# Kernel optimization log

Measured on AMD Instinct MI355X. Metric: run time of the kernel, lower is better.

Reference implementation:

```python
import jax, jax.numpy as jnp
import numpy as np

P = 4       # primitives
NF = 36     # non-functor cats (depth <= 1)
NEG = -1e9  # safe -inf
B, N, V, D = 32, 32, 32000, 64


def _build_functor_tables():
    # cat ids: 0..3 primitives; 4..35 depth-1 functors op(res,arg) res,arg<4;
    # remaining: depth-2 functors op(res,arg), res,arg in nf cats, not both primitive.
    def d1(op, res, arg):
        return 4 + op * 16 + res * 4 + arg
    nxt = NF
    d2 = {}
    for op in range(2):
        for res in range(NF):
            for arg in range(NF):
                if res < P and arg < P:
                    continue
                d2[(op, res, arg)] = nxt
                nxt += 1
    C = nxt  # 2596
    def fid(op, res, arg):
        return d1(op, res, arg) if (res < P and arg < P) else d2[(op, res, arg)]
    lf = np.zeros((NF, NF), np.int32)
    rf = np.zeros((NF, NF), np.int32)
    for res in range(NF):
        for arg in range(NF):
            lf[arg, res] = fid(0, res, arg)  # '-b' : functor on the left
            rf[arg, res] = fid(1, res, arg)  # '-a' : functor on the right
    return lf, rf, C


def setup_inputs() -> dict:
    lf, rf, C = _build_functor_tables()
    key = jax.random.key(0)
    ks = jax.random.split(key, 24)
    g = lambda i, shp, s: jax.random.normal(ks[i], shp, dtype=jnp.float32) * s
    inp = {
        "x": jax.random.randint(ks[0], (B, N), 0, V, dtype=jnp.int32),
        "l_functors": jnp.asarray(lf),
        "r_functors": jnp.asarray(rf),
        "root_W": g(1, (1, C), 0.1),
        "root_b": g(2, (C,), 0.1),
        "rule_W": g(3, (NF, 2 * NF), 0.1),
        "rule_b": g(4, (2 * NF,), 0.1),
        "nt_emb": g(5, (C, D), 1.0),
        "sW1": g(6, (D, D), 0.125), "sb1": g(7, (D,), 0.02),
        "r1W1": g(8, (D, D), 0.125), "r1b1": g(9, (D,), 0.02),
        "r1W2": g(10, (D, D), 0.125), "r1b2": g(11, (D,), 0.02),
        "r2W1": g(12, (D, D), 0.125), "r2b1": g(13, (D,), 0.02),
        "r2W2": g(14, (D, D), 0.125), "r2b2": g(15, (D,), 0.02),
        "sW2": g(16, (D, 2), 0.125), "sb2": g(17, (2,), 0.02),
        "vocab_W": g(18, (D, V), 0.125), "vocab_b": g(19, (V,), 0.02),
    }
    return inp


def _res_layer(h, W1, b1, W2, b2):
    return jax.nn.relu(jax.nn.relu(h @ W1 + b1) @ W2 + b2) + h


def reference(x, l_functors, r_functors, root_W, root_b, rule_W, rule_b, nt_emb,
              sW1, sb1, r1W1, r1b1, r1W2, r1b2, r2W1, r2b1, r2W2, r2b2,
              sW2, sb2, vocab_W, vocab_b):
    C = nt_emb.shape[0]
    # --- grammar parameters ---
    root_mask = jnp.where(jnp.arange(C) < P, 0.0, NEG)
    root_scores = jax.nn.log_softmax(root_mask + (root_W[0] + root_b))      # [C]
    rule_scores = jax.nn.log_softmax(rule_W + rule_b, axis=1)               # [NF,2NF] (rule_mlp(eye))
    h = nt_emb @ sW1 + sb1
    h = _res_layer(h, r1W1, r1b1, r1W2, r1b2)
    h = _res_layer(h, r2W1, r2b1, r2W2, r2b2)
    split = jax.nn.log_softmax(h @ sW2 + sb2, axis=1)                       # [C,2]
    G_larg = rule_scores[:, :NF] + split[:NF, 0:1]                          # [res,arg]
    G_rarg = rule_scores[:, NF:] + split[:NF, 0:1]
    # --- emission (word model): log_softmax over vocab, gather word ids ---
    dist = jax.nn.log_softmax(nt_emb @ vocab_W + vocab_b, axis=1)           # [C,V]
    emis = dist[:, x]                                                       # [C,B,N]
    beta1 = jnp.transpose(emis, (2, 1, 0)) + split[:, 1]                    # [N,B,C] lexical inside
    # --- CKY inside algorithm ---
    n = beta1.shape[0]
    lf_c = jnp.minimum(l_functors, NF - 1); l_valid = l_functors < NF
    rf_c = jnp.minimum(r_functors, NF - 1); r_valid = r_functors < NF
    rf1 = beta1[:, :, r_functors]   # [N,B,arg,res] functor score at length-1 spans
    lf1 = beta1[:, :, l_functors]
    Gl = G_larg.T                   # [arg,res]
    Gr = G_rarg.T
    chart = {1: beta1[:, :, :NF]}   # chart[L][i] = inside of span [i, i+L) over nf cats
    for L in range(2, n + 1):
        S = n - L + 1
        terms = []
        for k in range(1, L):  # left length k, right length L-k
            left = chart[k][:S]              # [S,B,NF]
            right = chart[L - k][k:k + S]    # [S,B,NF]
            # case larg: res -> arg (left, nf) + r_functor (right)
            if L - k == 1:
                rF = rf1[k:k + S]
            else:
                rF = jnp.where(r_valid, right[..., rf_c], NEG)
            tA = left[..., :, None] + rF + Gl                       # [S,B,arg,res]
            # case rarg: res -> l_functor (left) + arg (right, nf)
            if k == 1:
                lF = lf1[:S]
            else:
                lF = jnp.where(l_valid, left[..., lf_c], NEG)
            tB = right[..., :, None] + lF + Gr
            terms.append(jax.nn.logsumexp(jnp.concatenate([tA, tB], axis=2), axis=2))
        chart[L] = jax.nn.logsumexp(jnp.stack(terms, 0), axis=0)    # [S,B,NF]
    top = chart[n][0]                                               # [B,NF]
    logprob = jax.nn.logsumexp(top + root_scores[:NF], axis=-1)     # root mask keeps primitives only
    return -logprob
```

## Files before the change

kernel.cpp:

```cpp
#include <hip/hip_runtime.h>
#include <hip/hip_bf16.h>
#include <math.h>

#define CT 2596
#define NF36 36
#define BB 32
#define NN 32
#define VV 32000
#define DD 64
#define NEGF -1e9f
#define NVT 2000

typedef __attribute__((ext_vector_type(8))) short bf16x8;
typedef __attribute__((ext_vector_type(4))) float f32x4;

__device__ __forceinline__ uint32_t f2bf_bits(float x) {
  union { float f; uint32_t u; } v; v.f = x;
  return (v.u + 0x7FFFu + ((v.u >> 16) & 1u)) >> 16;
}
__device__ __forceinline__ float bflo(uint32_t u) {
  union { uint32_t u; float f; } v; v.u = u << 16; return v.f;
}
__device__ __forceinline__ float bfhi(uint32_t u) {
  union { uint32_t u; float f; } v; v.u = u & 0xFFFF0000u; return v.f;
}

__global__ __launch_bounds__(256) void k_mlp(
    const float* __restrict__ nt_emb,
    const float* __restrict__ sW1, const float* __restrict__ sb1,
    const float* __restrict__ r1W1, const float* __restrict__ r1b1,
    const float* __restrict__ r1W2, const float* __restrict__ r1b2,
    const float* __restrict__ r2W1, const float* __restrict__ r2b1,
    const float* __restrict__ r2W2, const float* __restrict__ r2b2,
    const float* __restrict__ sW2, const float* __restrict__ sb2,
    float* __restrict__ split0, float* __restrict__ split1) {
  int tid = threadIdx.x;
  int rl = tid >> 6, j = tid & 63;
  int c = blockIdx.x * 4 + rl;
  __shared__ float hs[4][64], ts[4][64];

  ts[rl][j] = nt_emb[(size_t)c * 64 + j];
  __syncthreads();
  float a = sb1[j];
  for (int i = 0; i < 64; i++) a += ts[rl][i] * sW1[i * 64 + j];
  __syncthreads();
  hs[rl][j] = a;
  __syncthreads();
  float u = r1b1[j];
  for (int i = 0; i < 64; i++) u += hs[rl][i] * r1W1[i * 64 + j];
  u = fmaxf(u, 0.f);
  ts[rl][j] = u;
  __syncthreads();
  float w = r1b2[j];
  for (int i = 0; i < 64; i++) w += ts[rl][i] * r1W2[i * 64 + j];
  w = fmaxf(w, 0.f) + hs[rl][j];
  __syncthreads();
  hs[rl][j] = w;
  __syncthreads();
  u = r2b1[j];
  for (int i = 0; i < 64; i++) u += hs[rl][i] * r2W1[i * 64 + j];
  u = fmaxf(u, 0.f);
  ts[rl][j] = u;
  __syncthreads();
  w = r2b2[j];
  for (int i = 0; i < 64; i++) w += ts[rl][i] * r2W2[i * 64 + j];
  w = fmaxf(w, 0.f) + hs[rl][j];
  __syncthreads();
  hs[rl][j] = w;
  __syncthreads();
  if (j < 2) {
    float o = sb2[j];
    for (int i = 0; i < 64; i++) o += hs[rl][i] * sW2[i * 2 + j];
    ts[rl][j] = o;
  }
  __syncthreads();
  if (j < 2) {
    float o0 = ts[rl][0], o1 = ts[rl][1];
    float mx = fmaxf(o0, o1);
    float l = mx + __logf(__expf(o0 - mx) + __expf(o1 - mx));
    if (j == 0) split0[c] = o0 - l;
    else        split1[c] = o1 - l;
  }
}

__global__ __launch_bounds__(256) void k_prelim(
    const float* __restrict__ rule_W, const float* __restrict__ rule_b,
    const float* __restrict__ root_W, const float* __restrict__ root_b,
    const float* __restrict__ split0,
    float* __restrict__ Gl, float* __restrict__ Gr, float* __restrict__ root36,
    float* __restrict__ lseacc) {
  __shared__ float rs[36 * 72];
  __shared__ float lse4s;
  int tid = threadIdx.x;
  for (int i = tid; i < CT; i += 256) lseacc[i] = 0.f;
  if (tid < 36) {
    float mx = -1e30f;
    for (int q = 0; q < 72; q++) mx = fmaxf(mx, rule_W[tid * 72 + q] + rule_b[q]);
    float ss = 0.f;
    for (int q = 0; q < 72; q++) ss += __expf(rule_W[tid * 72 + q] + rule_b[q] - mx);
    float l = mx + __logf(ss);
    for (int q = 0; q < 72; q++) rs[tid * 72 + q] = rule_W[tid * 72 + q] + rule_b[q] - l;
  }
  if (tid == 0) {
    float mx = -1e30f;
    for (int i = 0; i < 4; i++) mx = fmaxf(mx, root_W[i] + root_b[i]);
    float ss = 0.f;
    for (int i = 0; i < 4; i++) ss += __expf(root_W[i] + root_b[i] - mx);
    lse4s = mx + __logf(ss);
  }
  __syncthreads();
  if (tid < 36)
    root36[tid] = ((tid < 4) ? 0.f : NEGF) + root_W[tid] + root_b[tid] - lse4s;
  for (int i = tid; i < 1296; i += 256) {
    int arg = i / 36, res = i - arg * 36;
    float s0 = split0[res];
    Gl[i] = rs[res * 72 + arg] + s0;
    Gr[i] = rs[res * 72 + 36 + arg] + s0;
  }
}

__global__ __launch_bounds__(256) void k_cvt_w(
    const float* __restrict__ vocab_W, uint4* __restrict__ Wt) {
  int g = blockIdx.x * 256 + threadIdx.x;
  if (g >= NVT * 128) return;
  int l = g & 63;
  int f = (g >> 6) & 1;
  int vt = g >> 7;
  int v = vt * 16 + (l & 15);
  int kb = f * 32 + 8 * (l >> 4);
  uint32_t d[4];
#pragma unroll
  for (int p = 0; p < 4; p++) {
    float a = vocab_W[(size_t)(kb + 2 * p) * VV + v];
    float b = vocab_W[(size_t)(kb + 2 * p + 1) * VV + v];
    d[p] = f2bf_bits(a) | (f2bf_bits(b) << 16);
  }
  uint4 o; o.x = d[0]; o.y = d[1]; o.z = d[2]; o.w = d[3];
  Wt[g] = o;
}

__global__ __launch_bounds__(256) void k_gather_tok(
    const float* __restrict__ vocab_W, const float* __restrict__ vocab_b,
    const int* __restrict__ x, uint4* __restrict__ Bt, float* __restrict__ vbt) {
  int g = blockIdx.x * 256 + threadIdx.x;
  if (g >= 8192) return;
  int l = g & 63, kf = (g >> 6) & 1, t = g >> 7;
  int j = t * 16 + (l & 15);
  int tok = x[j];
  int kb = kf * 32 + 8 * (l >> 4);
  uint32_t d[4];
#pragma unroll
  for (int p = 0; p < 4; p++) {
    float a = vocab_W[(size_t)(kb + 2 * p) * VV + tok];
    float b = vocab_W[(size_t)(kb + 2 * p + 1) * VV + tok];
    d[p] = f2bf_bits(a) | (f2bf_bits(b) << 16);
  }
  uint4 o; o.x = d[0]; o.y = d[1]; o.z = d[2]; o.w = d[3];
  Bt[g] = o;
  if (g < 1024) vbt[g] = vocab_b[x[g]];
}

__global__ __launch_bounds__(256) void k_lse_mfma(
    const float* __restrict__ nt_emb, const uint4* __restrict__ Wt,
    const float* __restrict__ vocab_b, float* __restrict__ lseacc) {
  int tid = threadIdx.x;
  int w = tid >> 6, l = tid & 63;
  int c0 = blockIdx.y * 128;
  int lrow = l & 15, lgrp = l >> 4;

  bf16x8 A[8][2];
#pragma unroll
  for (int ct = 0; ct < 8; ct++) {
    int row = c0 + ct * 16 + lrow;
#pragma unroll
    for (int kf = 0; kf < 2; kf++) {
      bf16x8 fr;
      if (row < CT) {
        const float4* src = (const float4*)(nt_emb + (size_t)row * 64 + kf * 32 + lgrp * 8);
        float4 s0 = src[0], s1 = src[1];
        fr[0] = (short)f2bf_bits(s0.x); fr[1] = (short)f2bf_bits(s0.y);
        fr[2] = (short)f2bf_bits(s0.z); fr[3] = (short)f2bf_bits(s0.w);
        fr[4] = (short)f2bf_bits(s1.x); fr[5] = (short)f2bf_bits(s1.y);
        fr[6] = (short)f2bf_bits(s1.z); fr[7] = (short)f2bf_bits(s1.w);
      } else {
#pragma unroll
        for (int e = 0; e < 8; e++) fr[e] = 0;
      }
      A[ct][kf] = fr;
    }
  }

  float sums[8][4];
#pragma unroll
  for (int ct = 0; ct < 8; ct++)
#pragma unroll
    for (int i = 0; i < 4; i++) sums[ct][i] = 0.f;

  int t0 = blockIdx.x * 80;
  for (int t = t0 + w; t < t0 + 80; t += 4) {
    union { uint4 u; bf16x8 h; } b0, b1;
    b0.u = Wt[(size_t)(t * 2) * 64 + l];
    b1.u = Wt[(size_t)(t * 2 + 1) * 64 + l];
    float vb = vocab_b[t * 16 + lrow];
#pragma unroll
    for (int ct = 0; ct < 8; ct++) {
      f32x4 acc = {0.f, 0.f, 0.f, 0.f};
      acc = __builtin_amdgcn_mfma_f32_16x16x32_bf16(A[ct][0], b0.h, acc, 0, 0, 0);
      acc = __builtin_amdgcn_mfma_f32_16x16x32_bf16(A[ct][1], b1.h, acc, 0, 0, 0);
#pragma unroll
      for (int i = 0; i < 4; i++) sums[ct][i] += __expf(acc[i] + vb);
    }
  }

#pragma unroll
  for (int ct = 0; ct < 8; ct++)
#pragma unroll
    for (int i = 0; i < 4; i++) {
      float v = sums[ct][i];
      v += __shfl_xor(v, 1);
      v += __shfl_xor(v, 2);
      v += __shfl_xor(v, 4);
      v += __shfl_xor(v, 8);
      sums[ct][i] = v;
    }
  if (lrow == 0) {
#pragma unroll
    for (int ct = 0; ct < 8; ct++)
#pragma unroll
      for (int i = 0; i < 4; i++) {
        int row = c0 + ct * 16 + lgrp * 4 + i;
        if (row < CT) atomicAdd(&lseacc[row], sums[ct][i]);
      }
  }
}

__global__ __launch_bounds__(256) void k_beta1_mfma(
    const float* __restrict__ nt_emb, const uint4* __restrict__ Bt,
    const float* __restrict__ vbt, const float* __restrict__ lseacc,
    const float* __restrict__ split1, float* __restrict__ beta1) {
  int tid = threadIdx.x;
  int w = tid >> 6, l = tid & 63;
  int c0 = blockIdx.x * 64;
  int lrow = l & 15, lgrp = l >> 4;
  __shared__ float addS[64];
  if (tid < 64) {
    int row = c0 + tid;
    addS[tid] = (row < CT) ? (split1[row] - __logf(lseacc[row])) : 0.f;
  }

  bf16x8 A[4][2];
#pragma unroll
  for (int ct = 0; ct < 4; ct++) {
    int row = c0 + ct * 16 + lrow;
#pragma unroll
    for (int kf = 0; kf < 2; kf++) {
      bf16x8 fr;
      if (row < CT) {
        const float4* src = (const float4*)(nt_emb + (size_t)row * 64 + kf * 32 + lgrp * 8);
        float4 s0 = src[0], s1 = src[1];
        fr[0] = (short)f2bf_bits(s0.x); fr[1] = (short)f2bf_bits(s0.y);
        fr[2] = (short)f2bf_bits(s0.z); fr[3] = (short)f2bf_bits(s0.w);
        fr[4] = (short)f2bf_bits(s1.x); fr[5] = (short)f2bf_bits(s1.y);
        fr[6] = (short)f2bf_bits(s1.z); fr[7] = (short)f2bf_bits(s1.w);
      } else {
#pragma unroll
        for (int e = 0; e < 8; e++) fr[e] = 0;
      }
      A[ct][kf] = fr;
    }
  }
  __syncthreads();
  float addv[4][4];
#pragma unroll
  for (int ct = 0; ct < 4; ct++)
#pragma unroll
    for (int i = 0; i < 4; i++) addv[ct][i] = addS[ct * 16 + lgrp * 4 + i];

  for (int t = w; t < 64; t += 4) {
    union { uint4 u; bf16x8 h; } b0, b1;
    b0.u = Bt[t * 128 + l];
    b1.u = Bt[t * 128 + 64 + l];
    int j = t * 16 + lrow;
    float vb = vbt[j];
    int jc = (j & 31) * 32 + (j >> 5);
    float* outb = beta1 + (size_t)jc * CT;
#pragma unroll
    for (int ct = 0; ct < 4; ct++) {
      f32x4 acc = {0.f, 0.f, 0.f, 0.f};
      acc = __builtin_amdgcn_mfma_f32_16x16x32_bf16(A[ct][0], b0.h, acc, 0, 0, 0);
      acc = __builtin_amdgcn_mfma_f32_16x16x32_bf16(A[ct][1], b1.h, acc, 0, 0, 0);
      int r0 = c0 + ct * 16 + lgrp * 4;
      if (r0 + 3 < CT) {
        float4 o;
        o.x = acc[0] + vb + addv[ct][0];
        o.y = acc[1] + vb + addv[ct][1];
        o.z = acc[2] + vb + addv[ct][2];
        o.w = acc[3] + vb + addv[ct][3];
        *(float4*)(outb + r0) = o;
      } else {
        for (int i = 0; i < 4; i++)
          if (r0 + i < CT) outb[r0 + i] = acc[i] + vb + addv[ct][i];
      }
    }
  }
}

__global__ __launch_bounds__(256) void k_edge(
    const float* __restrict__ beta1, const int* __restrict__ lf_t,
    const int* __restrict__ rf_t, const float* __restrict__ Gl,
    const float* __restrict__ Gr,
    uint32_t* __restrict__ elB, uint32_t* __restrict__ erB) {
  int sb = blockIdx.x;
  const float* brow = beta1 + (size_t)sb * CT;
  size_t ob = (size_t)sb * 720;
  for (int wd = threadIdx.x; wd < 720; wd += 256) {
    int res = wd / 20, p = wd - res * 20;
    int a0 = 2 * p, a1 = 2 * p + 1;
    uint32_t l0 = 0, l1 = 0, r0 = 0, r1 = 0;
    if (a0 < 36) {
      int i0 = a0 * 36 + res;
      l0 = f2bf_bits(__expf(brow[lf_t[i0]] + Gr[i0]));
      r0 = f2bf_bits(__expf(brow[rf_t[i0]] + Gl[i0]));
    }
    if (a1 < 36) {
      int i1 = a1 * 36 + res;
      l1 = f2bf_bits(__expf(brow[lf_t[i1]] + Gr[i1]));
      r1 = f2bf_bits(__expf(brow[rf_t[i1]] + Gl[i1]));
    }
    elB[ob + wd] = l0 | (l1 << 16);
    erB[ob + wd] = r0 | (r1 << 16);
  }
}

__global__ __launch_bounds__(1024, 4) void k_cky(
    const float* __restrict__ beta1, const uint32_t* __restrict__ elB,
    const uint32_t* __restrict__ erB, const float* __restrict__ Gl,
    const float* __restrict__ Gr, const float* __restrict__ root36,
    float* __restrict__ out) {
  __shared__ __align__(16) float D[19008];
  __shared__ float Mt[528];
  __shared__ __align__(16) float PA[1280], PB[1280];
  __shared__ __align__(16) float Ec1lT[512], Ec1rT[512];
  __shared__ __align__(16) float eGlT[16], eGrT[16];
  __shared__ unsigned int candb[2][33];
  __shared__ float MIDacc[128];

  int b = blockIdx.x, tid = threadIdx.x;

  if (tid < 66) candb[tid / 33][tid % 33] = 0u;
  if (tid < 32) Mt[tid] = 0.f;
  if (tid < 16) {
    int res = tid >> 2, a = tid & 3;
    eGlT[tid] = __expf(Gl[a * 36 + res]);
    eGrT[tid] = __expf(Gr[a * 36 + res]);
  }
  for (int i = tid; i < 1280; i += 1024) { PA[i] = 0.f; PB[i] = 0.f; }
  __syncthreads();
  for (int i = tid; i < 32 * 36; i += 1024) {
    int s = i / 36;
    float v = __expf(beta1[(size_t)(s * 32 + b) * CT + (i - s * 36)]);
    D[i] = v;
    atomicMax(&candb[1][s], __float_as_uint(v));
  }
  __syncthreads();
  for (int i = tid; i < 512; i += 1024) {
    int s = i >> 4, rr = (i >> 2) & 3, a = i & 3;
    float d1 = D[s * 36 + a];
    Ec1lT[i] = d1 * eGlT[rr * 4 + a];
    Ec1rT[i] = d1 * eGrT[rr * 4 + a];
  }
  __syncthreads();

  for (int L = 2; L <= 32; L++) {
    int S = 33 - L;
    int offL  = 36 * (((L - 1) * (66 - L)) >> 1);
    int offP  = 36 * (((L - 2) * (67 - L)) >> 1);
    int offML = ((L - 1) * (66 - L)) >> 1;
    int offMP = ((L - 2) * (67 - L)) >> 1;
    int par = L & 1, parP = par ^ 1;

    if (tid < 33) candb[par][tid] = 0u;
    if (tid >= 64 && tid < 192) MIDacc[tid - 64] = 0.f;
    int totA = S * 36;
    for (int o = tid; o < totA; o += 1024) {
      int s = o / 36, j = o - s * 36;
      float MtA = Mt[offMP + s], MtB = Mt[offMP + s + 1];
      float cA = MtA + __logf(fmaxf(__uint_as_float(candb[parP][s]), 1e-37f));
      float cB = MtB + __logf(fmaxf(__uint_as_float(candb[parP][s + 1]), 1e-37f));
      float Mn = fmaxf(cA, cB);
      PA[s * 40 + j] = D[offP + s * 36 + j] * __expf(MtA - Mn);
      PB[s * 40 + j] = D[offP + (s + 1) * 36 + j] * __expf(MtB - Mn);
      if (j == 0) Mt[offML + s] = Mn;
    }
    __syncthreads();

    int tot = S * 36;
    int nmid = (L >= 4) ? 4 * S * (L - 3) : 0;
    int W = tot + nmid;
    for (int o = tid; o < W; o += 1024) {
      if (o < tot) {
        int s = o / 36, res = o - s * 36;
        const uint4* el4 = (const uint4*)(elB + (size_t)(s * 32 + b) * 720 + res * 20);
        const uint4* er4 = (const uint4*)(erB + (size_t)((s + L - 1) * 32 + b) * 720 + res * 20);
        const float4* pB4 = (const float4*)(PB + s * 40);
        const float4* pA4 = (const float4*)(PA + s * 40);
        float a0 = 0.f, a1 = 0.f, a2 = 0.f, a3 = 0.f;
#pragma unroll
        for (int q = 0; q < 5; q++) {
          uint4 u = el4[q];
          float4 p0 = pB4[2 * q], p1 = pB4[2 * q + 1];
          a0 = fmaf(bflo(u.x), p0.x, a0); a1 = fmaf(bfhi(u.x), p0.y, a1);
          a2 = fmaf(bflo(u.y), p0.z, a2); a3 = fmaf(bfhi(u.y), p0.w, a3);
          a0 = fmaf(bflo(u.z), p1.x, a0); a1 = fmaf(bfhi(u.z), p1.y, a1);
          a2 = fmaf(bflo(u.w), p1.z, a2); a3 = fmaf(bfhi(u.w), p1.w, a3);
          uint4 v = er4[q];
          float4 q0 = pA4[2 * q], q1 = pA4[2 * q + 1];
          a0 = fmaf(bflo(v.x), q0.x, a0); a1 = fmaf(bfhi(v.x), q0.y, a1);
          a2 = fmaf(bflo(v.y), q0.z, a2); a3 = fmaf(bfhi(v.y), q0.w, a3);
          a0 = fmaf(bflo(v.z), q1.x, a0); a1 = fmaf(bfhi(v.z), q1.y, a1);
          a2 = fmaf(bflo(v.w), q1.z, a2); a3 = fmaf(bfhi(v.w), q1.w, a3);
        }
        if (res < 4 && L >= 3) {
          const float4* ecl = (const float4*)(Ec1lT + s * 16 + res * 4);
          const float4* ecr = (const float4*)(Ec1rT + (s + L - 1) * 16 + res * 4);
          float4 e0 = ecl[0], pb = pB4[5 + res];
          float4 e1 = ecr[0], pa = pA4[1 + res];
          a0 = fmaf(e0.x, pb.x, a0); a1 = fmaf(e0.y, pb.y, a1);
          a2 = fmaf(e0.z, pb.z, a2); a3 = fmaf(e0.w, pb.w, a3);
          a0 = fmaf(e1.x, pa.x, a0); a1 = fmaf(e1.y, pa.y, a1);
          a2 = fmaf(e1.z, pa.z, a2); a3 = fmaf(e1.w, pa.w, a3);
        }
        float val = (a0 + a1) + (a2 + a3);
        D[offL + o] = val;
        atomicMax(&candb[par][s], __float_as_uint(val));
      } else {
        int o2 = o - tot;
        int kidx = o2 / (4 * S);
        int rem = o2 - kidx * 4 * S;
        int s = rem >> 2, res = rem & 3;
        int k = kidx + 2;
        int lk = L - k;
        int tk = ((k - 1) * (66 - k)) >> 1;
        int tl = ((lk - 1) * (66 - lk)) >> 1;
        const float4* Dk4 = (const float4*)(D + 36 * tk + s * 36);
        const float4* Dl4 = (const float4*)(D + 36 * tl + (s + k) * 36);
        float4 dk0 = Dk4[0], dkh = Dk4[1 + res];
        float4 dl0 = Dl4[0], dlh = Dl4[5 + res];
        float4 egl = ((const float4*)eGlT)[res];
        float4 egr = ((const float4*)eGrT)[res];
        float f = __expf(Mt[tk + s] + Mt[tl + s + k] - Mt[offML + s]);
        float sub = dk0.x * dlh.x * egl.x + dk0.y * dlh.y * egl.y
                  + dk0.z * dlh.z * egl.z + dk0.w * dlh.w * egl.w
                  + dl0.x * dkh.x * egr.x + dl0.y * dkh.y * egr.y
                  + dl0.z * dkh.z * egr.z + dl0.w * dkh.w * egr.w;
        atomicAdd(&MIDacc[rem], f * sub);
      }
    }
    __syncthreads();

    if (L >= 4) {
      for (int o = tid; o < 4 * S; o += 1024) {
        int s = o >> 2;
        float nv = D[offL + s * 36 + (o & 3)] + MIDacc[o];
        D[offL + s * 36 + (o & 3)] = nv;
        atomicMax(&candb[par][s], __float_as_uint(nv));
      }
    }
    __syncthreads();
  }

  int wid = tid >> 6, lane = tid & 63;
  if (wid == 0) {
    int off32 = 36 * ((31 * 34) >> 1);
    float v = (lane < 36) ? D[off32 + lane] * __expf(root36[lane]) : 0.f;
#pragma unroll
    for (int w = 32; w > 0; w >>= 1) v += __shfl_xor(v, w);
    if (lane == 0) out[b] = -(Mt[527] + __logf(v));
  }
}

extern "C" void kernel_launch(void* const* d_in, const int* in_sizes, int n_in,
                              void* d_out, int out_size, void* d_ws, size_t ws_size,
                              hipStream_t stream) {
  const int*   x       = (const int*)d_in[0];
  const int*   lf_t    = (const int*)d_in[1];
  const int*   rf_t    = (const int*)d_in[2];
  const float* root_W  = (const float*)d_in[3];
  const float* root_b  = (const float*)d_in[4];
  const float* rule_W  = (const float*)d_in[5];
  const float* rule_b  = (const float*)d_in[6];
  const float* nt_emb  = (const float*)d_in[7];
  const float* sW1     = (const float*)d_in[8];
  const float* sb1     = (const float*)d_in[9];
  const float* r1W1    = (const float*)d_in[10];
  const float* r1b1    = (const float*)d_in[11];
  const float* r1W2    = (const float*)d_in[12];
  const float* r1b2    = (const float*)d_in[13];
  const float* r2W1    = (const float*)d_in[14];
  const float* r2b1    = (const float*)d_in[15];
  const float* r2W2    = (const float*)d_in[16];
  const float* r2b2    = (const float*)d_in[17];
  const float* sW2     = (const float*)d_in[18];
  const float* sb2     = (const float*)d_in[19];
  const float* vocab_W = (const float*)d_in[20];
  const float* vocab_b = (const float*)d_in[21];
  float* outp = (float*)d_out;

  float* ws = (float*)d_ws;
  float* split0 = ws;
  float* split1 = ws + 2596;
  float* Gl     = ws + 5192;
  float* Gr     = ws + 6488;
  float* root36 = ws + 7784;
  float* lseacc = ws + 7848;
  float* vbt    = ws + 10448;
  float* beta1  = ws + 11472;
  uint32_t* elB = (uint32_t*)(ws + 2669776);
  uint32_t* erB = (uint32_t*)(ws + 3407056);
  uint4* Wt     = (uint4*)(ws + 2669776);
  uint4* Bt     = (uint4*)(ws + 4144336);

  k_mlp<<<649, 256, 0, stream>>>(nt_emb, sW1, sb1, r1W1, r1b1, r1W2, r1b2,
                                 r2W1, r2b1, r2W2, r2b2, sW2, sb2, split0, split1);
  k_prelim<<<1, 256, 0, stream>>>(rule_W, rule_b, root_W, root_b, split0,
                                  Gl, Gr, root36, lseacc);
  k_cvt_w<<<1000, 256, 0, stream>>>(vocab_W, Wt);
  k_gather_tok<<<32, 256, 0, stream>>>(vocab_W, vocab_b, x, Bt, vbt);
  k_lse_mfma<<<dim3(25, 21), 256, 0, stream>>>(nt_emb, Wt, vocab_b, lseacc);
  k_beta1_mfma<<<41, 256, 0, stream>>>(nt_emb, Bt, vbt, lseacc, split1, beta1);
  k_edge<<<1024, 256, 0, stream>>>(beta1, lf_t, rf_t, Gl, Gr, elB, erB);
  k_cky<<<32, 1024, 0, stream>>>(beta1, elB, erB, Gl, Gr, root36, outp);
}
```

Before: 228.4 us.

## Parallelize prelim, merge prep kernels, split beta1 grid, defer CKY mid-term fold

k_prelim is spread over 37 blocks, one per rule row plus one for the root, instead of running in a single block. The weight-convert, token-gather and lseacc-zeroing kernels are merged into one launch, and k_beta1_mfma gets an 8-way grid split over token tiles. In k_cky the separate pass that folds MIDacc into the chart is removed: the fold now happens lazily in the next length's normalisation step, using double-buffered MIDacc and a compact C4 copy of primitive cells, which drops one block-wide barrier per span length. The edge-weight loads are also prefetched into registers before the first barrier, at the cost of extra register pressure and more complex max tracking.

```diff
diff --git a/kernel.cpp b/kernel.cpp
--- a/kernel.cpp
+++ b/kernel.cpp
@@ -83,81 +83,88 @@
   }
 }
 
-__global__ __launch_bounds__(256) void k_prelim(
+__global__ __launch_bounds__(128) void k_prelim(
     const float* __restrict__ rule_W, const float* __restrict__ rule_b,
     const float* __restrict__ root_W, const float* __restrict__ root_b,
     const float* __restrict__ split0,
-    float* __restrict__ Gl, float* __restrict__ Gr, float* __restrict__ root36,
+    float* __restrict__ Gl, float* __restrict__ Gr, float* __restrict__ root36) {
+  int tid = threadIdx.x;
+  int blk = blockIdx.x;
+  if (blk < 36) {
+    int res = blk;
+    __shared__ float red[4];
+    float v = (tid < 72) ? rule_W[res * 72 + tid] + rule_b[tid] : -1e30f;
+    float m = v;
+#pragma unroll
+    for (int w = 32; w > 0; w >>= 1) m = fmaxf(m, __shfl_xor(m, w));
+    if ((tid & 63) == 0) red[tid >> 6] = m;
+    __syncthreads();
+    m = fmaxf(red[0], red[1]);
+    float e = (tid < 72) ? __expf(v - m) : 0.f;
+#pragma unroll
+    for (int w = 32; w > 0; w >>= 1) e += __shfl_xor(e, w);
+    if ((tid & 63) == 0) red[2 + (tid >> 6)] = e;
+    __syncthreads();
+    float l = m + __logf(red[2] + red[3]);
+    if (tid < 36) {
+      float s0 = split0[res];
+      Gl[tid * 36 + res] = rule_W[res * 72 + tid] + rule_b[tid] - l + s0;
+      Gr[tid * 36 + res] = rule_W[res * 72 + 36 + tid] + rule_b[36 + tid] - l + s0;
+    }
+  } else {
+    __shared__ float lse4s;
+    if (tid == 0) {
+      float mx = -1e30f;
+      for (int i = 0; i < 4; i++) mx = fmaxf(mx, root_W[i] + root_b[i]);
+      float ss = 0.f;
+      for (int i = 0; i < 4; i++) ss += __expf(root_W[i] + root_b[i] - mx);
+      lse4s = mx + __logf(ss);
+    }
+    __syncthreads();
+    if (tid < 36)
+      root36[tid] = ((tid < 4) ? 0.f : NEGF) + root_W[tid] + root_b[tid] - lse4s;
+  }
+}
+
+__global__ __launch_bounds__(256) void k_prep(
+    const float* __restrict__ vocab_W, const float* __restrict__ vocab_b,
+    const int* __restrict__ x, uint4* __restrict__ Wt,
+    uint4* __restrict__ Bt, float* __restrict__ vbt,
     float* __restrict__ lseacc) {
-  __shared__ float rs[36 * 72];
-  __shared__ float lse4s;
-  int tid = threadIdx.x;
-  for (int i = tid; i < CT; i += 256) lseacc[i] = 0.f;
-  if (tid < 36) {
-    float mx = -1e30f;
-    for (int q = 0; q < 72; q++) mx = fmaxf(mx, rule_W[tid * 72 + q] + rule_b[q]);
-    float ss = 0.f;
-    for (int q = 0; q < 72; q++) ss += __expf(rule_W[tid * 72 + q] + rule_b[q] - mx);
-    float l = mx + __logf(ss);
-    for (int q = 0; q < 72; q++) rs[tid * 72 + q] = rule_W[tid * 72 + q] + rule_b[q] - l;
-  }
-  if (tid == 0) {
-    float mx = -1e30f;
-    for (int i = 0; i < 4; i++) mx = fmaxf(mx, root_W[i] + root_b[i]);
-    float ss = 0.f;
-    for (int i = 0; i < 4; i++) ss += __expf(root_W[i] + root_b[i] - mx);
-    lse4s = mx + __logf(ss);
-  }
-  __syncthreads();
-  if (tid < 36)
-    root36[tid] = ((tid < 4) ? 0.f : NEGF) + root_W[tid] + root_b[tid] - lse4s;
-  for (int i = tid; i < 1296; i += 256) {
-    int arg = i / 36, res = i - arg * 36;
-    float s0 = split0[res];
-    Gl[i] = rs[res * 72 + arg] + s0;
-    Gr[i] = rs[res * 72 + 36 + arg] + s0;
-  }
-}
-
-__global__ __launch_bounds__(256) void k_cvt_w(
-    const float* __restrict__ vocab_W, uint4* __restrict__ Wt) {
-  int g = blockIdx.x * 256 + threadIdx.x;
-  if (g >= NVT * 128) return;
-  int l = g & 63;
-  int f = (g >> 6) & 1;
-  int vt = g >> 7;
-  int v = vt * 16 + (l & 15);
-  int kb = f * 32 + 8 * (l >> 4);
-  uint32_t d[4];
-#pragma unroll
-  for (int p = 0; p < 4; p++) {
-    float a = vocab_W[(size_t)(kb + 2 * p) * VV + v];
-    float b = vocab_W[(size_t)(kb + 2 * p + 1) * VV + v];
-    d[p] = f2bf_bits(a) | (f2bf_bits(b) << 16);
-  }
-  uint4 o; o.x = d[0]; o.y = d[1]; o.z = d[2]; o.w = d[3];
-  Wt[g] = o;
-}
-
-__global__ __launch_bounds__(256) void k_gather_tok(
-    const float* __restrict__ vocab_W, const float* __restrict__ vocab_b,
-    const int* __restrict__ x, uint4* __restrict__ Bt, float* __restrict__ vbt) {
-  int g = blockIdx.x * 256 + threadIdx.x;
-  if (g >= 8192) return;
-  int l = g & 63, kf = (g >> 6) & 1, t = g >> 7;
-  int j = t * 16 + (l & 15);
-  int tok = x[j];
-  int kb = kf * 32 + 8 * (l >> 4);
-  uint32_t d[4];
-#pragma unroll
-  for (int p = 0; p < 4; p++) {
-    float a = vocab_W[(size_t)(kb + 2 * p) * VV + tok];
-    float b = vocab_W[(size_t)(kb + 2 * p + 1) * VV + tok];
-    d[p] = f2bf_bits(a) | (f2bf_bits(b) << 16);
-  }
-  uint4 o; o.x = d[0]; o.y = d[1]; o.z = d[2]; o.w = d[3];
-  Bt[g] = o;
-  if (g < 1024) vbt[g] = vocab_b[x[g]];
+  int blk = blockIdx.x;
+  if (blk < 1000) {
+    int g = blk * 256 + threadIdx.x;
+    int l = g & 63, f = (g >> 6) & 1, vt = g >> 7;
+    int v = vt * 16 + (l & 15);
+    int kb = f * 32 + 8 * (l >> 4);
+    uint32_t d[4];
+#pragma unroll
+    for (int p = 0; p < 4; p++) {
+      float a = vocab_W[(size_t)(kb + 2 * p) * VV + v];
+      float b = vocab_W[(size_t)(kb + 2 * p + 1) * VV + v];
+      d[p] = f2bf_bits(a) | (f2bf_bits(b) << 16);
+    }
+    uint4 o; o.x = d[0]; o.y = d[1]; o.z = d[2]; o.w = d[3];
+    Wt[g] = o;
+  } else if (blk < 1032) {
+    int g = (blk - 1000) * 256 + threadIdx.x;
+    int l = g & 63, kf = (g >> 6) & 1, t = g >> 7;
+    int j = t * 16 + (l & 15);
+    int tok = x[j];
+    int kb = kf * 32 + 8 * (l >> 4);
+    uint32_t d[4];
+#pragma unroll
+    for (int p = 0; p < 4; p++) {
+      float a = vocab_W[(size_t)(kb + 2 * p) * VV + tok];
+      float b = vocab_W[(size_t)(kb + 2 * p + 1) * VV + tok];
+      d[p] = f2bf_bits(a) | (f2bf_bits(b) << 16);
+    }
+    uint4 o; o.x = d[0]; o.y = d[1]; o.z = d[2]; o.w = d[3];
+    Bt[g] = o;
+    if (g < 1024) vbt[g] = vocab_b[x[g]];
+  } else {
+    for (int i = threadIdx.x; i < CT; i += 256) lseacc[i] = 0.f;
+  }
 }
 
 __global__ __launch_bounds__(256) void k_lse_mfma(
@@ -276,7 +283,8 @@
 #pragma unroll
     for (int i = 0; i < 4; i++) addv[ct][i] = addS[ct * 16 + lgrp * 4 + i];
 
-  for (int t = w; t < 64; t += 4) {
+  int t0 = blockIdx.y * 8;
+  for (int t = t0 + w; t < t0 + 8; t += 4) {
     union { uint4 u; bf16x8 h; } b0, b1;
     b0.u = Bt[t * 128 + l];
     b1.u = Bt[t * 128 + 64 + l];
@@ -338,12 +346,13 @@
     const float* __restrict__ Gr, const float* __restrict__ root36,
     float* __restrict__ out) {
   __shared__ __align__(16) float D[19008];
+  __shared__ __align__(16) float C4[2116];
   __shared__ float Mt[528];
   __shared__ __align__(16) float PA[1280], PB[1280];
   __shared__ __align__(16) float Ec1lT[512], Ec1rT[512];
   __shared__ __align__(16) float eGlT[16], eGrT[16];
   __shared__ unsigned int candb[2][33];
-  __shared__ float MIDacc[128];
+  __shared__ float MIDacc[2][128];
 
   int b = blockIdx.x, tid = threadIdx.x;
 
@@ -372,48 +381,81 @@
   __syncthreads();
 
   for (int L = 2; L <= 32; L++) {
-    int S = 33 - L;
-    int offL  = 36 * (((L - 1) * (66 - L)) >> 1);
-    int offP  = 36 * (((L - 2) * (67 - L)) >> 1);
-    int offML = ((L - 1) * (66 - L)) >> 1;
-    int offMP = ((L - 2) * (67 - L)) >> 1;
-    int par = L & 1, parP = par ^ 1;
+    const int S = 33 - L;
+    const int offL  = 36 * (((L - 1) * (66 - L)) >> 1);
+    const int offP  = 36 * (((L - 2) * (67 - L)) >> 1);
+    const int offML = ((L - 1) * (66 - L)) >> 1;
+    const int offMP = ((L - 2) * (67 - L)) >> 1;
+    const int par = L & 1, parP = par ^ 1;
+    const int tot = S * 36;
+    const int nmid = (L >= 4) ? 4 * S * (L - 3) : 0;
+    const int W = tot + nmid;
+
+    uint4 pl[5], pr[5];
+    if (tid < tot) {
+      int s = tid / 36, res = tid - s * 36;
+      const uint4* el4 = (const uint4*)(elB + (size_t)(s * 32 + b) * 720 + res * 20);
+      const uint4* er4 = (const uint4*)(erB + (size_t)((s + L - 1) * 32 + b) * 720 + res * 20);
+#pragma unroll
+      for (int q = 0; q < 5; q++) { pl[q] = el4[q]; pr[q] = er4[q]; }
+    }
 
     if (tid < 33) candb[par][tid] = 0u;
-    if (tid >= 64 && tid < 192) MIDacc[tid - 64] = 0.f;
-    int totA = S * 36;
-    for (int o = tid; o < totA; o += 1024) {
+    if (tid >= 512 && tid < 640) MIDacc[par][tid - 512] = 0.f;
+    const float* MIDp = MIDacc[parP];
+    for (int o = tid; o < tot; o += 1024) {
       int s = o / 36, j = o - s * 36;
       float MtA = Mt[offMP + s], MtB = Mt[offMP + s + 1];
-      float cA = MtA + __logf(fmaxf(__uint_as_float(candb[parP][s]), 1e-37f));
-      float cB = MtB + __logf(fmaxf(__uint_as_float(candb[parP][s + 1]), 1e-37f));
+      float dA = D[offP + s * 36 + j];
+      float dB = D[offP + (s + 1) * 36 + j];
+      if (L >= 5 && j < 4) { dA += MIDp[s * 4 + j]; dB += MIDp[(s + 1) * 4 + j]; }
+      if (j < 4) {
+        C4[(offMP + s) * 4 + j] = dA;
+        if (s == S - 1) C4[(offMP + s + 1) * 4 + j] = dB;
+      }
+      float mA = __uint_as_float(candb[parP][s]);
+      float mB = __uint_as_float(candb[parP][s + 1]);
+      if (L >= 5) {
+#pragma unroll
+        for (int j2 = 0; j2 < 4; j2++) {
+          mA = fmaxf(mA, D[offP + s * 36 + j2] + MIDp[s * 4 + j2]);
+          mB = fmaxf(mB, D[offP + (s + 1) * 36 + j2] + MIDp[(s + 1) * 4 + j2]);
+        }
+      }
+      float cA = MtA + __logf(fmaxf(mA, 1e-37f));
+      float cB = MtB + __logf(fmaxf(mB, 1e-37f));
       float Mn = fmaxf(cA, cB);
-      PA[s * 40 + j] = D[offP + s * 36 + j] * __expf(MtA - Mn);
-      PB[s * 40 + j] = D[offP + (s + 1) * 36 + j] * __expf(MtB - Mn);
+      PA[s * 40 + j] = dA * __expf(MtA - Mn);
+      PB[s * 40 + j] = dB * __expf(MtB - Mn);
       if (j == 0) Mt[offML + s] = Mn;
     }
     __syncthreads();
 
-    int tot = S * 36;
-    int nmid = (L >= 4) ? 4 * S * (L - 3) : 0;
-    int W = tot + nmid;
     for (int o = tid; o < W; o += 1024) {
       if (o < tot) {
         int s = o / 36, res = o - s * 36;
-        const uint4* el4 = (const uint4*)(elB + (size_t)(s * 32 + b) * 720 + res * 20);
-        const uint4* er4 = (const uint4*)(erB + (size_t)((s + L - 1) * 32 + b) * 720 + res * 20);
+        uint4 u5[5], v5[5];
+        if (o == tid) {
+#pragma unroll
+          for (int q = 0; q < 5; q++) { u5[q] = pl[q]; v5[q] = pr[q]; }
+        } else {
+          const uint4* el4 = (const uint4*)(elB + (size_t)(s * 32 + b) * 720 + res * 20);
+          const uint4* er4 = (const uint4*)(erB + (size_t)((s + L - 1) * 32 + b) * 720 + res * 20);
+#pragma unroll
+          for (int q = 0; q < 5; q++) { u5[q] = el4[q]; v5[q] = er4[q]; }
+        }
         const float4* pB4 = (const float4*)(PB + s * 40);
         const float4* pA4 = (const float4*)(PA + s * 40);
         float a0 = 0.f, a1 = 0.f, a2 = 0.f, a3 = 0.f;
 #pragma unroll
         for (int q = 0; q < 5; q++) {
-          uint4 u = el4[q];
+          uint4 u = u5[q];
           float4 p0 = pB4[2 * q], p1 = pB4[2 * q + 1];
           a0 = fmaf(bflo(u.x), p0.x, a0); a1 = fmaf(bfhi(u.x), p0.y, a1);
           a2 = fmaf(bflo(u.y), p0.z, a2); a3 = fmaf(bfhi(u.y), p0.w, a3);
           a0 = fmaf(bflo(u.z), p1.x, a0); a1 = fmaf(bfhi(u.z), p1.y, a1);
           a2 = fmaf(bflo(u.w), p1.z, a2); a3 = fmaf(bfhi(u.w), p1.w, a3);
-          uint4 v = er4[q];
+          uint4 v = v5[q];
           float4 q0 = pA4[2 * q], q1 = pA4[2 * q + 1];
           a0 = fmaf(bflo(v.x), q0.x, a0); a1 = fmaf(bfhi(v.x), q0.y, a1);
           a2 = fmaf(bflo(v.y), q0.z, a2); a3 = fmaf(bfhi(v.y), q0.w, a3);
@@ -438,14 +480,15 @@
         int kidx = o2 / (4 * S);
         int rem = o2 - kidx * 4 * S;
         int s = rem >> 2, res = rem & 3;
-        int k = kidx + 2;
-        int lk = L - k;
+        int k = kidx + 2, lk = L - k;
         int tk = ((k - 1) * (66 - k)) >> 1;
         int tl = ((lk - 1) * (66 - lk)) >> 1;
-        const float4* Dk4 = (const float4*)(D + 36 * tk + s * 36);
-        const float4* Dl4 = (const float4*)(D + 36 * tl + (s + k) * 36);
-        float4 dk0 = Dk4[0], dkh = Dk4[1 + res];
-        float4 dl0 = Dl4[0], dlh = Dl4[5 + res];
+        float4 dk0 = *(const float4*)(C4 + (tk + s) * 4);
+        float4 dl0 = *(const float4*)(C4 + (tl + s + k) * 4);
+        const float4* Dk4 = (const float4*)(D + (tk + s) * 36);
+        const float4* Dl4 = (const float4*)(D + (tl + s + k) * 36);
+        float4 dkh = Dk4[1 + res];
+        float4 dlh = Dl4[5 + res];
         float4 egl = ((const float4*)eGlT)[res];
         float4 egr = ((const float4*)eGrT)[res];
         float f = __expf(Mt[tk + s] + Mt[tl + s + k] - Mt[offML + s]);
@@ -453,17 +496,7 @@
                   + dk0.z * dlh.z * egl.z + dk0.w * dlh.w * egl.w
                   + dl0.x * dkh.x * egr.x + dl0.y * dkh.y * egr.y
                   + dl0.z * dkh.z * egr.z + dl0.w * dkh.w * egr.w;
-        atomicAdd(&MIDacc[rem], f * sub);
-      }
-    }
-    __syncthreads();
-
-    if (L >= 4) {
-      for (int o = tid; o < 4 * S; o += 1024) {
-        int s = o >> 2;
-        float nv = D[offL + s * 36 + (o & 3)] + MIDacc[o];
-        D[offL + s * 36 + (o & 3)] = nv;
-        atomicMax(&candb[par][s], __float_as_uint(nv));
+        atomicAdd(&MIDacc[par][rem], f * sub);
       }
     }
     __syncthreads();
@@ -472,7 +505,8 @@
   int wid = tid >> 6, lane = tid & 63;
   if (wid == 0) {
     int off32 = 36 * ((31 * 34) >> 1);
-    float v = (lane < 36) ? D[off32 + lane] * __expf(root36[lane]) : 0.f;
+    float add = (lane < 4) ? MIDacc[0][lane] : 0.f;
+    float v = (lane < 36) ? (D[off32 + lane] + add) * __expf(root36[lane]) : 0.f;
 #pragma unroll
     for (int w = 32; w > 0; w >>= 1) v += __shfl_xor(v, w);
     if (lane == 0) out[b] = -(Mt[527] + __logf(v));
@@ -522,12 +556,11 @@
 
   k_mlp<<<649, 256, 0, stream>>>(nt_emb, sW1, sb1, r1W1, r1b1, r1W2, r1b2,
                                  r2W1, r2b1, r2W2, r2b2, sW2, sb2, split0, split1);
-  k_prelim<<<1, 256, 0, stream>>>(rule_W, rule_b, root_W, root_b, split0,
-                                  Gl, Gr, root36, lseacc);
-  k_cvt_w<<<1000, 256, 0, stream>>>(vocab_W, Wt);
-  k_gather_tok<<<32, 256, 0, stream>>>(vocab_W, vocab_b, x, Bt, vbt);
+  k_prelim<<<37, 128, 0, stream>>>(rule_W, rule_b, root_W, root_b, split0,
+                                   Gl, Gr, root36);
+  k_prep<<<1033, 256, 0, stream>>>(vocab_W, vocab_b, x, Wt, Bt, vbt, lseacc);
   k_lse_mfma<<<dim3(25, 21), 256, 0, stream>>>(nt_emb, Wt, vocab_b, lseacc);
-  k_beta1_mfma<<<41, 256, 0, stream>>>(nt_emb, Bt, vbt, lseacc, split1, beta1);
+  k_beta1_mfma<<<dim3(41, 8), 256, 0, stream>>>(nt_emb, Bt, vbt, lseacc, split1, beta1);
   k_edge<<<1024, 256, 0, stream>>>(beta1, lf_t, rf_t, Gl, Gr, elB, erB);
   k_cky<<<32, 1024, 0, stream>>>(beta1, elB, erB, Gl, Gr, root36, outp);
 }
```

Result: slower. 346.3 us (+51.6%).
